# Kernel optimization log

Hardware: AMD Instinct MI355X
Metric: run time of the kernel (lower is better)

The kernel has to match this reference:

```python
import jax, jax.numpy as jnp
import numpy as np

B, T, NF, C, H, TOPK = 4, 8, 8192, 384, 12, 32
D = C // H
SCALE = D ** -0.5  # qk_scale=None -> head_dim**-0.5


def setup_inputs() -> dict:
    key = jax.random.key(0)
    ks = jax.random.split(key, 4)
    x = jax.random.normal(ks[0], (B, T + NF, C), jnp.float32)
    qs_w = jax.random.normal(ks[1], (T, C, C), jnp.float32) * (C ** -0.5)
    kv_w = jax.random.normal(ks[2], (C, 2 * C), jnp.float32) * (C ** -0.5)
    experts_w = jax.random.normal(ks[3], (T, C, C), jnp.float32) * (C ** -0.5)
    return {"x": x, "qs_w": qs_w, "kv_w": kv_w, "experts_w": experts_w}


def reference(x, qs_w, kv_w, experts_w):
    # x: [B, T+NF, C]; first T tokens are task tokens, rest are feature tokens
    feature = x[:, T:, :]                                          # [B,NF,C]
    kv = (feature @ kv_w).reshape(B, NF, 2, H, D)                  # out dim splits [2,H,D]
    k = kv[:, :, 0].transpose(0, 2, 1, 3)                          # [B,H,NF,D]
    v = kv[:, :, 1].transpose(0, 2, 1, 3)                          # [B,H,NF,D]
    # per-task query linears (no bias), one task token each
    q = jnp.einsum('btc,tco->bto', x[:, :T, :], qs_w)              # [B,T,C]
    q = q.reshape(B, T, H, D).transpose(0, 2, 1, 3)                # [B,H,T,D]
    attn = jnp.einsum('bhtd,bhnd->bhtn', q, k) * SCALE             # [B,H,T,NF]
    vals, idx = jax.lax.top_k(attn, TOPK)                          # [B,H,T,K]
    w = jax.nn.softmax(vals, axis=-1)                              # softmax over top-k only
    # attn_token = (scatter(topk softmax) @ v) == weighted gather of v rows
    v_g = jnp.take_along_axis(v[:, :, None], idx[..., None], axis=3)   # [B,H,T,K,D]
    attn_token = jnp.einsum('bhtk,bhtkd->bhtd', w, v_g)
    attn_token = attn_token.transpose(0, 2, 1, 3).reshape(B, T, C)     # [B,T,C]
    # gather raw feature tokens at top-k indices, weight, scatter into padded zeros
    fm = feature.reshape(B, NF, H, D).transpose(0, 2, 1, 3)        # [B,H,NF,D]
    f_g = jnp.take_along_axis(fm[:, :, None], idx[..., None], axis=3) * w[..., None]  # [B,H,T,K,D]
    bi = jnp.arange(B)[:, None, None, None]
    hi = jnp.arange(H)[None, :, None, None]
    ti = jnp.arange(T)[None, None, :, None]
    # topk indices are unique per row -> set is well-defined
    feature_pad = jnp.zeros((B, H, T, NF, D), x.dtype).at[bi, hi, ti, idx].set(f_g)
    feature_pad = feature_pad.transpose(0, 2, 3, 1, 4).reshape(B, T, NF, C)  # [B,T,NF,C]
    # per-task expert linears; einsum with ones weight == sum over tasks
    feature_out = jnp.einsum('btnc,tco->bno', feature_pad, experts_w)  # [B,NF,C]
    token_out = jnp.einsum('btc,tco->bto', attn_token, experts_w)      # [B,T,C]
    return jnp.concatenate([token_out, feature_out], axis=1)          # [B,T+NF,C]
```

## Files before the change

kernel.cpp:

```cpp
#include <hip/hip_runtime.h>
#include <hip/hip_bf16.h>
#include <math.h>

#define B 4
#define T 8
#define NF 8192
#define C 384
#define H 12
#define TOPK 32
#define D 32
#define STOT (T + NF)
#define R (H * T)
#define KSEL 48
#define SCALE 0.17677669529663687f

typedef unsigned int uint;
typedef unsigned short ushort;
typedef short bf16x8 __attribute__((ext_vector_type(8)));
typedef float f32x4 __attribute__((ext_vector_type(4)));

__device__ __forceinline__ ushort bf16u(float a) {
  return __builtin_bit_cast(ushort, __float2bfloat16(a));
}

__device__ __forceinline__ ushort f32_key(float s) {
  uint kb = bf16u(s);
  kb ^= (kb & 0x8000u) ? 0xFFFFu : 0x8000u;
  return (ushort)kb;
}

__global__ __launch_bounds__(256) void ta_qproj_kernel(
    const float* __restrict__ x, const float* __restrict__ qs_w,
    float* __restrict__ q_part) {
  int t = blockIdx.x;
  int o0 = blockIdx.y * 64;
  int z = blockIdx.z;
  int tid = threadIdx.x;
  int o = tid & 63, ks = tid >> 6;
  __shared__ float xs[B][192];
  __shared__ float part[4][B][64];
  if (tid < 192) {
    int b = tid / 48, j4 = (tid % 48) * 4;
    *reinterpret_cast<float4*>(&xs[b][j4]) =
        *reinterpret_cast<const float4*>(x + ((size_t)b * STOT + t) * C + z * 192 + j4);
  }
  __syncthreads();
  float a0 = 0.f, a1 = 0.f, a2 = 0.f, a3 = 0.f;
  const float* w = qs_w + (size_t)t * C * C + (size_t)(z * 192 + ks * 48) * C + o0 + o;
#pragma unroll 8
  for (int c = 0; c < 48; ++c) {
    float wv = w[(size_t)c * C];
    int cj = ks * 48 + c;
    a0 += xs[0][cj] * wv;
    a1 += xs[1][cj] * wv;
    a2 += xs[2][cj] * wv;
    a3 += xs[3][cj] * wv;
  }
  part[ks][0][o] = a0; part[ks][1][o] = a1;
  part[ks][2][o] = a2; part[ks][3][o] = a3;
  __syncthreads();
  {
    int b = tid >> 6, oo = tid & 63;
    float s = part[0][b][oo] + part[1][b][oo] + part[2][b][oo] + part[3][b][oo];
    q_part[(((size_t)z * B + b) * T + t) * C + o0 + oo] = s;
  }
}

__global__ __launch_bounds__(384) void ta_fold_kernel(
    const float* __restrict__ q_part, const float* __restrict__ kv_w,
    float* __restrict__ qk_f32, ushort* __restrict__ qk_bf) {
  int b = blockIdx.x / H, h = blockIdx.x % H;
  int tid = threadIdx.x;
  __shared__ float kS[C][33];
  __shared__ float qh[T][D];
  if (tid < T * D) {
    int t = tid >> 5, d = tid & 31;
    qh[t][d] = q_part[((size_t)b * T + t) * C + h * D + d] +
               q_part[(((size_t)B + b) * T + t) * C + h * D + d];
  }
  for (int j = tid; j < C * 8; j += 384) {
    int c = j >> 3, d4 = (j & 7) * 4;
    float4 v = *reinterpret_cast<const float4*>(
        kv_w + (size_t)c * (2 * C) + h * D + d4);
    kS[c][d4 + 0] = v.x; kS[c][d4 + 1] = v.y;
    kS[c][d4 + 2] = v.z; kS[c][d4 + 3] = v.w;
  }
  __syncthreads();
  float acc[T] = {0.f, 0.f, 0.f, 0.f, 0.f, 0.f, 0.f, 0.f};
#pragma unroll
  for (int d = 0; d < D; ++d) {
    float kv = kS[tid][d];
#pragma unroll
    for (int t = 0; t < T; ++t) acc[t] += qh[t][d] * kv;
  }
#pragma unroll
  for (int t = 0; t < T; ++t) {
    size_t off = ((size_t)b * R + (size_t)h * T + t) * C + tid;
    float a = acc[t];
    qk_f32[off] = a;
    qk_bf[off] = bf16u(a);
  }
}

__global__ __launch_bounds__(256) void ta_scores_kernel(
    const float* __restrict__ x, const ushort* __restrict__ qk_bf,
    ushort* __restrict__ keys, float4* __restrict__ out4) {
  int b = blockIdx.y;
  int n0 = blockIdx.x * 64;
  int tid = threadIdx.x;
  int lane = tid & 63, w = tid >> 6;
  int row16 = lane & 15, kg = lane >> 4;
  __shared__ ushort fS[64][72];
  __shared__ ushort qS[96][72];
  f32x4 acc[6];
#pragma unroll
  for (int i = 0; i < 6; ++i) acc[i] = (f32x4){0.f, 0.f, 0.f, 0.f};

  {
    const int SL = (B * STOT * C / 4) / 512;
    int zbid = blockIdx.y * gridDim.x + blockIdx.x;
    float4 z = {0.f, 0.f, 0.f, 0.f};
    float4* dst = out4 + (size_t)zbid * SL;
    for (int j = tid; j < SL; j += 256) dst[j] = z;
  }

  const float* xb = x + ((size_t)b * STOT + T + n0) * C;
  const ushort* qb = qk_bf + (size_t)b * R * C;

  int frow = tid >> 2, fcg = (tid & 3) * 8;

#pragma unroll 1
  for (int c0 = 0; c0 < C; c0 += 32) {
    {
      const float* src = xb + (size_t)frow * C + c0 + fcg;
      float4 v0 = *reinterpret_cast<const float4*>(src);
      float4 v1 = *reinterpret_cast<const float4*>(src + 4);
      uint4 p;
      p.x = (uint)bf16u(v0.x) | ((uint)bf16u(v0.y) << 16);
      p.y = (uint)bf16u(v0.z) | ((uint)bf16u(v0.w) << 16);
      p.z = (uint)bf16u(v1.x) | ((uint)bf16u(v1.y) << 16);
      p.w = (uint)bf16u(v1.z) | ((uint)bf16u(v1.w) << 16);
      *reinterpret_cast<uint4*>(&fS[frow][fcg]) = p;
    }
#pragma unroll
    for (int s = 0; s < 2; ++s) {
      int u = tid + 256 * s;
      if (u < 384) {
        int row = u >> 2, cg = (u & 3) * 8;
        uint4 v = *reinterpret_cast<const uint4*>(qb + (size_t)row * C + c0 + cg);
        *reinterpret_cast<uint4*>(&qS[row][cg]) = v;
      }
    }
    __syncthreads();
    bf16x8 bfr = *reinterpret_cast<const bf16x8*>(&fS[w * 16 + row16][kg * 8]);
#pragma unroll
    for (int i = 0; i < 6; ++i) {
      bf16x8 afr = *reinterpret_cast<const bf16x8*>(&qS[i * 16 + row16][kg * 8]);
      acc[i] = __builtin_amdgcn_mfma_f32_16x16x32_bf16(afr, bfr, acc[i], 0, 0, 0);
    }
    __syncthreads();
  }
  int n = n0 + w * 16 + row16;
#pragma unroll
  for (int i = 0; i < 6; ++i) {
    int rbase = i * 16 + kg * 4;
#pragma unroll
    for (int reg = 0; reg < 4; ++reg) {
      keys[((size_t)b * R + rbase + reg) * NF + n] = f32_key(acc[i][reg] * SCALE);
    }
  }
}

__global__ __launch_bounds__(384) void ta_seltail_kernel(
    const ushort* __restrict__ keys, const float* __restrict__ x,
    const float* __restrict__ qk_f32, const float* __restrict__ kv_w,
    const float* __restrict__ ew, float* __restrict__ out) {
  int rr = blockIdx.x;
  int t = rr % T, h = (rr / T) % H, b = rr / R;
  int hD = h * D;
  int tid = threadIdx.x;
  int lane = tid & 63, wvi = tid >> 6;

  union SM {
    struct {
      uint hist[4096];
      uint cand[1024];
    } s;
    struct {
      float fbarS[C];
      float gS[TOPK][D];
      float part[8][D];
    } g;
  };
  __shared__ SM sm;
  __shared__ __align__(16) ushort su[NF];
  __shared__ uint wtot[4];
  __shared__ uint sh_piv, cnt;
  __shared__ int il[KSEL];
  __shared__ float sv[KSEL];
  __shared__ int rkS[KSEL];
  __shared__ float qS[C];
  __shared__ float wl[TOPK];
  __shared__ int top_il[TOPK];
  __shared__ __align__(16) float attS[D];
  __shared__ float smax, esum;

  {
    const uint4* src = reinterpret_cast<const uint4*>(keys + (size_t)rr * NF);
    uint4* dst = reinterpret_cast<uint4*>(su);
    for (int j = tid; j < NF / 8; j += 384) dst[j] = src[j];
  }
  qS[tid] = qk_f32[(size_t)rr * C + tid];
  {
    uint4 z4 = {0u, 0u, 0u, 0u};
    uint4* hz = reinterpret_cast<uint4*>(sm.s.hist);
    for (int i = tid; i < 1024; i += 384) hz[i] = z4;
  }
  if (tid == 0) cnt = 0;
  __syncthreads();

  for (int i = tid; i < NF; i += 384) atomicAdd(&sm.s.hist[su[i] >> 4], 1u);
  __syncthreads();

  uint pp = 0, suf = 0;
  if (tid < 256) {
#pragma unroll
    for (int j = 0; j < 16; ++j) pp += sm.s.hist[tid * 16 + j];
    suf = pp;
#pragma unroll
    for (int off = 1; off < 64; off <<= 1) {
      uint o = __shfl_down(suf, off);
      if (lane + off < 64) suf += o;
    }
    if (lane == 0) wtot[wvi] = suf;
  }
  __syncthreads();
  if (tid < 256) {
    uint later = 0;
    for (int wq = wvi + 1; wq < 4; ++wq) later += wtot[wq];
    uint geg = later + suf;
    uint gng = geg - pp;
    if (geg >= (uint)KSEL && gng < (uint)KSEL) {
      uint run = gng;
      int pv = 0;
      for (int j = 15; j >= 0; --j) {
        uint c = sm.s.hist[tid * 16 + j];
        uint nrun = run + c;
        if (nrun >= (uint)KSEL && run < (uint)KSEL) pv = tid * 16 + j;
        run = nrun;
      }
      sh_piv = (uint)pv;
    }
  }
  __syncthreads();
  uint piv = sh_piv;
  for (int i = tid; i < NF; i += 384) {
    uint u = su[i];
    if ((u >> 4) >= piv) {
      uint s = atomicAdd(&cnt, 1u);
      if (s < 1024) sm.s.cand[s] = (u << 13) | (8191u - (uint)i);
    }
  }
  __syncthreads();
  {
    uint m = cnt < 1024u ? cnt : 1024u;
    if (tid < (int)m) {
      uint me = sm.s.cand[tid];
      int r = 0;
      for (uint e = 0; e < m; ++e) r += (sm.s.cand[e] > me);
      if (r < KSEL) il[r] = 8191 - (int)(me & 8191u);
    }
  }
  __syncthreads();

  {
    int k = tid >> 3, j = tid & 7;
    const float* fp = x + ((size_t)b * STOT + T + il[k]) * C + j;
    float s = 0.f;
#pragma unroll 8
    for (int m2 = 0; m2 < 48; ++m2) s += fp[m2 * 8] * qS[j + m2 * 8];
    s += __shfl_down(s, 4);
    s += __shfl_down(s, 2);
    s += __shfl_down(s, 1);
    if (j == 0) sv[k] = s * SCALE;
  }
  __syncthreads();
  if (tid < KSEL) {
    float mys = sv[tid];
    int myn = il[tid];
    int r = 0;
#pragma unroll
    for (int e = 0; e < KSEL; ++e) {
      float se = sv[e];
      r += (se > mys) || (se == mys && il[e] < myn);
    }
    rkS[tid] = r;
    if (r == 0) smax = mys;
  }
  __syncthreads();
  {
    float e = 0.f;
    if (tid < KSEL && rkS[tid] < TOPK) e = expf(sv[tid] - smax);
    if (tid < 64) {
      float t2 = e;
#pragma unroll
      for (int off = 32; off; off >>= 1) t2 += __shfl_down(t2, off);
      if (tid == 0) esum = t2;
    }
    __syncthreads();
    if (tid < KSEL && rkS[tid] < TOPK) {
      wl[rkS[tid]] = e / esum;
      top_il[rkS[tid]] = il[tid];
    }
  }
  __syncthreads();

  {
    float fbar = 0.f;
    bool ing = (tid >= hD) && (tid < hD + D);
#pragma unroll 4
    for (int k = 0; k < TOPK; ++k) {
      float v = x[((size_t)b * STOT + T + top_il[k]) * C + tid];
      float wv = wl[k] * v;
      fbar += wv;
      if (ing) sm.g.gS[k][tid - hD] = wv;
    }
    sm.g.fbarS[tid] = fbar;
  }
  __syncthreads();

  if (tid < 256) {
    int d = tid & 31, seg = tid >> 5;
    const float* vw = kv_w + C + hD + d;
    float a0 = 0.f, a1 = 0.f;
    int cb = seg * 48;
#pragma unroll 8
    for (int c = 0; c < 48; c += 2) {
      a0 += sm.g.fbarS[cb + c] * vw[(size_t)(cb + c) * (2 * C)];
      a1 += sm.g.fbarS[cb + c + 1] * vw[(size_t)(cb + c + 1) * (2 * C)];
    }
    sm.g.part[seg][d] = a0 + a1;
  }
  __syncthreads();
  if (tid < D) {
    float a = 0.f;
#pragma unroll
    for (int s = 0; s < 8; ++s) a += sm.g.part[s][tid];
    attS[tid] = a;
  }
  __syncthreads();

  float ewc[D];
  const float* ewt = ew + (size_t)t * C * C + (size_t)hD * C + tid;
#pragma unroll
  for (int dd = 0; dd < D; ++dd) ewc[dd] = ewt[(size_t)dd * C];
  size_t obase = (size_t)b * STOT * C + tid;
#pragma unroll 1
  for (int kk = 0; kk < TOPK; ++kk) {
    float y = 0.f;
#pragma unroll
    for (int d4 = 0; d4 < D; d4 += 4) {
      float4 g4 = *reinterpret_cast<const float4*>(&sm.g.gS[kk][d4]);
      y += g4.x * ewc[d4] + g4.y * ewc[d4 + 1] +
           g4.z * ewc[d4 + 2] + g4.w * ewc[d4 + 3];
    }
    atomicAdd(&out[obase + (size_t)(T + top_il[kk]) * C], y);
  }
  {
    float y = 0.f;
#pragma unroll
    for (int d4 = 0; d4 < D; d4 += 4) {
      float4 a4 = *reinterpret_cast<const float4*>(attS + d4);
      y += a4.x * ewc[d4] + a4.y * ewc[d4 + 1] +
           a4.z * ewc[d4 + 2] + a4.w * ewc[d4 + 3];
    }
    atomicAdd(&out[obase + (size_t)t * C], y);
  }
}

extern "C" void kernel_launch(void* const* d_in, const int* in_sizes, int n_in,
                              void* d_out, int out_size, void* d_ws, size_t ws_size,
                              hipStream_t stream) {
  const float* x = (const float*)d_in[0];
  const float* qs_w = (const float*)d_in[1];
  const float* kv_w = (const float*)d_in[2];
  const float* ew = (const float*)d_in[3];
  float* out = (float*)d_out;

  char* p = (char*)d_ws;
  float* qk_f32 = (float*)p;  p += (size_t)B * R * C * 4;
  ushort* qk_bf = (ushort*)p; p += (size_t)B * R * C * 2;
  ushort* keys = (ushort*)p;  p += (size_t)B * R * NF * 2;
  float* q_part = (float*)p;

  dim3 gq(T, C / 64, 2);
  ta_qproj_kernel<<<gq, 256, 0, stream>>>(x, qs_w, q_part);
  ta_fold_kernel<<<B * H, 384, 0, stream>>>(q_part, kv_w, qk_f32, qk_bf);
  dim3 g2(NF / 64, B);
  ta_scores_kernel<<<g2, 256, 0, stream>>>(x, qk_bf, keys, (float4*)out);
  ta_seltail_kernel<<<B * R, 384, 0, stream>>>(keys, x, qk_f32, kv_w, ew, out);
}
```

Measured before the change: 79.96 us.

## Split top-k selection into per-chunk selection kernel plus merge-tail kernel

The per-row selection over all 8192 keys moves out of the single tail kernel into a new kernel that processes 4 chunks per row. Each chunk builds its own histogram, finds a pivot, and writes its local top-48 candidates to a workspace buffer. A new merge kernel ranks the 192 candidates per row and then runs the original gather, softmax and expert tail. The aim is to raise block-level parallelism from one block per row to four and shrink per-block shared memory. The cost is an extra kernel launch and a global round trip for the candidates. The chunk-level rank step is quadratic in the number of candidates, so many ties in the pivot bin could make it slow.

```diff
diff --git a/kernel.cpp b/kernel.cpp
--- a/kernel.cpp
+++ b/kernel.cpp
@@ -12,6 +12,8 @@
 #define STOT (T + NF)
 #define R (H * T)
 #define KSEL 48
+#define NCH 4
+#define CHSZ (NF / NCH)
 #define SCALE 0.17677669529663687f
 
 typedef unsigned int uint;
@@ -171,71 +173,39 @@
   }
 }
 
-__global__ __launch_bounds__(384) void ta_seltail_kernel(
-    const ushort* __restrict__ keys, const float* __restrict__ x,
-    const float* __restrict__ qk_f32, const float* __restrict__ kv_w,
-    const float* __restrict__ ew, float* __restrict__ out) {
-  int rr = blockIdx.x;
-  int t = rr % T, h = (rr / T) % H, b = rr / R;
-  int hD = h * D;
+__global__ __launch_bounds__(256) void ta_selchunk_kernel(
+    const ushort* __restrict__ keys, uint* __restrict__ cand_buf) {
+  int ch = blockIdx.x, rr = blockIdx.y;
   int tid = threadIdx.x;
   int lane = tid & 63, wvi = tid >> 6;
-
-  union SM {
-    struct {
-      uint hist[4096];
-      uint cand[1024];
-    } s;
-    struct {
-      float fbarS[C];
-      float gS[TOPK][D];
-      float part[8][D];
-    } g;
-  };
-  __shared__ SM sm;
-  __shared__ __align__(16) ushort su[NF];
+  __shared__ uint hist[4096];
+  __shared__ uint cand[CHSZ];
   __shared__ uint wtot[4];
   __shared__ uint sh_piv, cnt;
-  __shared__ int il[KSEL];
-  __shared__ float sv[KSEL];
-  __shared__ int rkS[KSEL];
-  __shared__ float qS[C];
-  __shared__ float wl[TOPK];
-  __shared__ int top_il[TOPK];
-  __shared__ __align__(16) float attS[D];
-  __shared__ float smax, esum;
-
-  {
-    const uint4* src = reinterpret_cast<const uint4*>(keys + (size_t)rr * NF);
-    uint4* dst = reinterpret_cast<uint4*>(su);
-    for (int j = tid; j < NF / 8; j += 384) dst[j] = src[j];
-  }
-  qS[tid] = qk_f32[(size_t)rr * C + tid];
+  const ushort* kp = keys + (size_t)rr * NF + (size_t)ch * CHSZ;
+
   {
     uint4 z4 = {0u, 0u, 0u, 0u};
-    uint4* hz = reinterpret_cast<uint4*>(sm.s.hist);
-    for (int i = tid; i < 1024; i += 384) hz[i] = z4;
+    uint4* hz = reinterpret_cast<uint4*>(hist);
+    for (int i = tid; i < 1024; i += 256) hz[i] = z4;
   }
   if (tid == 0) cnt = 0;
   __syncthreads();
-
-  for (int i = tid; i < NF; i += 384) atomicAdd(&sm.s.hist[su[i] >> 4], 1u);
-  __syncthreads();
-
-  uint pp = 0, suf = 0;
-  if (tid < 256) {
-#pragma unroll
-    for (int j = 0; j < 16; ++j) pp += sm.s.hist[tid * 16 + j];
-    suf = pp;
-#pragma unroll
-    for (int off = 1; off < 64; off <<= 1) {
-      uint o = __shfl_down(suf, off);
-      if (lane + off < 64) suf += o;
-    }
-    if (lane == 0) wtot[wvi] = suf;
-  }
-  __syncthreads();
-  if (tid < 256) {
+  for (int i = tid; i < CHSZ; i += 256) atomicAdd(&hist[kp[i] >> 4], 1u);
+  __syncthreads();
+
+  uint pp = 0;
+#pragma unroll
+  for (int j = 0; j < 16; ++j) pp += hist[tid * 16 + j];
+  uint suf = pp;
+#pragma unroll
+  for (int off = 1; off < 64; off <<= 1) {
+    uint o = __shfl_down(suf, off);
+    if (lane + off < 64) suf += o;
+  }
+  if (lane == 0) wtot[wvi] = suf;
+  __syncthreads();
+  {
     uint later = 0;
     for (int wq = wvi + 1; wq < 4; ++wq) later += wtot[wq];
     uint geg = later + suf;
@@ -244,7 +214,7 @@
       uint run = gng;
       int pv = 0;
       for (int j = 15; j >= 0; --j) {
-        uint c = sm.s.hist[tid * 16 + j];
+        uint c = hist[tid * 16 + j];
         uint nrun = run + c;
         if (nrun >= (uint)KSEL && run < (uint)KSEL) pv = tid * 16 + j;
         run = nrun;
@@ -254,22 +224,54 @@
   }
   __syncthreads();
   uint piv = sh_piv;
-  for (int i = tid; i < NF; i += 384) {
-    uint u = su[i];
+  for (int i = tid; i < CHSZ; i += 256) {
+    uint u = kp[i];
     if ((u >> 4) >= piv) {
       uint s = atomicAdd(&cnt, 1u);
-      if (s < 1024) sm.s.cand[s] = (u << 13) | (8191u - (uint)i);
-    }
-  }
-  __syncthreads();
-  {
-    uint m = cnt < 1024u ? cnt : 1024u;
-    if (tid < (int)m) {
-      uint me = sm.s.cand[tid];
-      int r = 0;
-      for (uint e = 0; e < m; ++e) r += (sm.s.cand[e] > me);
-      if (r < KSEL) il[r] = 8191 - (int)(me & 8191u);
-    }
+      cand[s] = (u << 13) | (8191u - (uint)(ch * CHSZ + i));
+    }
+  }
+  __syncthreads();
+  uint m = cnt;
+  for (int i2 = tid; i2 < (int)m; i2 += 256) {
+    uint me = cand[i2];
+    int r = 0;
+    for (uint e = 0; e < m; ++e) r += (cand[e] > me);
+    if (r < KSEL) cand_buf[((size_t)rr * NCH + ch) * KSEL + r] = me;
+  }
+}
+
+__global__ __launch_bounds__(384) void ta_mergetail_kernel(
+    const uint* __restrict__ cand_buf, const float* __restrict__ x,
+    const float* __restrict__ qk_f32, const float* __restrict__ kv_w,
+    const float* __restrict__ ew, float* __restrict__ out) {
+  constexpr int M = NCH * KSEL;
+  int rr = blockIdx.x;
+  int t = rr % T, h = (rr / T) % H, b = rr / R;
+  int hD = h * D;
+  int tid = threadIdx.x;
+  __shared__ uint candS[M];
+  __shared__ int il[KSEL];
+  __shared__ float sv[KSEL];
+  __shared__ int rkS[KSEL];
+  __shared__ float qS[C];
+  __shared__ float wl[TOPK];
+  __shared__ int top_il[TOPK];
+  __shared__ float fbarS[C];
+  __shared__ float gS[TOPK][D];
+  __shared__ float part[8][D];
+  __shared__ __align__(16) float attS[D];
+  __shared__ float smax, esum;
+
+  if (tid < M) candS[tid] = cand_buf[(size_t)rr * M + tid];
+  qS[tid] = qk_f32[(size_t)rr * C + tid];
+  __syncthreads();
+  if (tid < M) {
+    uint me = candS[tid];
+    int r = 0;
+#pragma unroll 8
+    for (int e = 0; e < M; ++e) r += (candS[e] > me);
+    if (r < KSEL) il[r] = 8191 - (int)(me & 8191u);
   }
   __syncthreads();
 
@@ -323,9 +325,9 @@
       float v = x[((size_t)b * STOT + T + top_il[k]) * C + tid];
       float wv = wl[k] * v;
       fbar += wv;
-      if (ing) sm.g.gS[k][tid - hD] = wv;
-    }
-    sm.g.fbarS[tid] = fbar;
+      if (ing) gS[k][tid - hD] = wv;
+    }
+    fbarS[tid] = fbar;
   }
   __syncthreads();
 
@@ -336,16 +338,16 @@
     int cb = seg * 48;
 #pragma unroll 8
     for (int c = 0; c < 48; c += 2) {
-      a0 += sm.g.fbarS[cb + c] * vw[(size_t)(cb + c) * (2 * C)];
-      a1 += sm.g.fbarS[cb + c + 1] * vw[(size_t)(cb + c + 1) * (2 * C)];
-    }
-    sm.g.part[seg][d] = a0 + a1;
+      a0 += fbarS[cb + c] * vw[(size_t)(cb + c) * (2 * C)];
+      a1 += fbarS[cb + c + 1] * vw[(size_t)(cb + c + 1) * (2 * C)];
+    }
+    part[seg][d] = a0 + a1;
   }
   __syncthreads();
   if (tid < D) {
     float a = 0.f;
 #pragma unroll
-    for (int s = 0; s < 8; ++s) a += sm.g.part[s][tid];
+    for (int s = 0; s < 8; ++s) a += part[s][tid];
     attS[tid] = a;
   }
   __syncthreads();
@@ -360,7 +362,7 @@
     float y = 0.f;
 #pragma unroll
     for (int d4 = 0; d4 < D; d4 += 4) {
-      float4 g4 = *reinterpret_cast<const float4*>(&sm.g.gS[kk][d4]);
+      float4 g4 = *reinterpret_cast<const float4*>(&gS[kk][d4]);
       y += g4.x * ewc[d4] + g4.y * ewc[d4 + 1] +
            g4.z * ewc[d4 + 2] + g4.w * ewc[d4 + 3];
     }
@@ -391,6 +393,7 @@
   float* qk_f32 = (float*)p;  p += (size_t)B * R * C * 4;
   ushort* qk_bf = (ushort*)p; p += (size_t)B * R * C * 2;
   ushort* keys = (ushort*)p;  p += (size_t)B * R * NF * 2;
+  uint* cand_buf = (uint*)p;  p += (size_t)B * R * NCH * KSEL * 4;
   float* q_part = (float*)p;
 
   dim3 gq(T, C / 64, 2);
@@ -398,5 +401,7 @@
   ta_fold_kernel<<<B * H, 384, 0, stream>>>(q_part, kv_w, qk_f32, qk_bf);
   dim3 g2(NF / 64, B);
   ta_scores_kernel<<<g2, 256, 0, stream>>>(x, qk_bf, keys, (float4*)out);
-  ta_seltail_kernel<<<B * R, 384, 0, stream>>>(keys, x, qk_f32, kv_w, ew, out);
-}
+  dim3 gs(NCH, B * R);
+  ta_selchunk_kernel<<<gs, 256, 0, stream>>>(keys, cand_buf);
+  ta_mergetail_kernel<<<B * R, 384, 0, stream>>>(cand_buf, x, qk_f32, kv_w, ew, out);
+}
```

Measured after the change: 83.81 us. 1.05x slower.
